# Kernel tuning notes

Hardware: AMD Instinct MI355X
Metric: run time of the kernel (lower is better)

Reference implementation:

```python
import jax, jax.numpy as jnp
import numpy as np

B, S, E, H = 2, 2048, 1024, 16
D = E // H  # head_dim = 64


def setup_inputs() -> dict:
    key = jax.random.key(0)
    ks = jax.random.split(key, 8)
    lim = float(np.sqrt(6.0 / (E + E)))  # xavier_uniform
    inp = {
        "query": jax.random.normal(ks[0], (B, S, E), jnp.float32),
        "key": jax.random.normal(ks[1], (B, S, E), jnp.float32),
        "value": jax.random.normal(ks[2], (B, S, E), jnp.float32),
        "Wq": jax.random.uniform(ks[3], (E, E), jnp.float32, -lim, lim),
        "Wk": jax.random.uniform(ks[4], (E, E), jnp.float32, -lim, lim),
        "Wv": jax.random.uniform(ks[5], (E, E), jnp.float32, -lim, lim),
        "Wo": jax.random.uniform(ks[6], (E, E), jnp.float32, -lim, lim),
        "bq": jnp.zeros((E,), jnp.float32),
        "bk": jnp.zeros((E,), jnp.float32),
        "bv": jnp.zeros((E,), jnp.float32),
        "bo": jnp.zeros((E,), jnp.float32),
        # causal mask: True = masked (strictly upper triangular)
        "attn_mask": jnp.triu(jnp.ones((S, S), jnp.bool_), k=1),
    }
    return inp


def reference(query, key, value, Wq, Wk, Wv, Wo, bq, bk, bv, bo, attn_mask):
    # W stored as (in, out); torch Linear equivalent y = x @ W + b
    scaling = D ** (-0.5)
    q = (query @ Wq + bq) * scaling            # (B,S,E), first scaling (MHA.forward)
    k = key @ Wk + bk
    v = value @ Wv + bv
    # split heads -> (B, H, S, D)
    q = q.reshape(B, S, H, D).transpose(0, 2, 1, 3)
    k = k.reshape(B, S, H, D).transpose(0, 2, 1, 3)
    v = v.reshape(B, S, H, D).transpose(0, 2, 1, 3)
    # second scaling inside ScaledDotProductAttention (faithful double-scale)
    scores = jnp.einsum("bhqd,bhkd->bhqk", q, k) / jnp.sqrt(jnp.float32(D))
    scores = jnp.where(attn_mask[None, None, :, :], -jnp.inf, scores)
    attn = jax.nn.softmax(scores, axis=-1)     # dropout is identity in eval
    out = jnp.einsum("bhqk,bhkd->bhqd", attn, v)
    out = out.transpose(0, 2, 1, 3).reshape(B, S, E)
    return out @ Wo + bo
```

## Files before the change

kernel.cpp:

```cpp
#include <hip/hip_runtime.h>
#include <stdint.h>

#define B_ 2
#define S_ 2048
#define E_ 1024
#define H_ 16
#define D_ 64

typedef __attribute__((ext_vector_type(8))) short bf16x8;
typedef __attribute__((ext_vector_type(4))) float f32x4;
typedef __attribute__((ext_vector_type(4))) short s16x4_t;

__device__ __forceinline__ short bfbits(float x) {
    union { float f; uint32_t u; } v; v.f = x;
    uint32_t r = v.u + 0x7fffu + ((v.u >> 16) & 1u);
    return (short)(r >> 16);
}
__device__ __forceinline__ short bfbits_trunc(float x) {
    union { float f; uint32_t u; } v; v.f = x;
    return (short)(v.u >> 16);
}

__device__ __forceinline__ void async16(const short* g, short* l) {
    __builtin_amdgcn_global_load_lds((const __attribute__((address_space(1))) void*)g,
                                     (__attribute__((address_space(3))) void*)l,
                                     16, 0, 0);
}

__global__ __launch_bounds__(256) void cvt_all(const float* __restrict__ q,
                                               const float* __restrict__ k,
                                               const float* __restrict__ v,
                                               const float* __restrict__ Wq,
                                               const float* __restrict__ Wk,
                                               const float* __restrict__ Wv,
                                               const float* __restrict__ Wo,
                                               short* __restrict__ dstX,
                                               short* __restrict__ dstW) {
    __shared__ short t[64][72];
    int bid = blockIdx.x;
    if (bid < 12288) {
        const long long NV = 1048576;
        long long i = (long long)bid * 256 + threadIdx.x;
        const float* src = (i < NV) ? q : (i < 2 * NV) ? k : v;
        long long j = (i >= 2 * NV) ? (i - 2 * NV) : (i >= NV) ? (i - NV) : i;
        float4 x = ((const float4*)src)[j];
        s16x4_t o;
        o[0] = bfbits(x.x); o[1] = bfbits(x.y); o[2] = bfbits(x.z); o[3] = bfbits(x.w);
        ((s16x4_t*)dstX)[i] = o;
        return;
    }
    int wbid = bid - 12288;
    int z = wbid >> 8;
    const float* W = (z == 0) ? Wq : (z == 1) ? Wk : (z == 2) ? Wv : Wo;
    short* o = dstW + (size_t)z * 1048576;
    int rem = wbid & 255;
    int n0 = (rem & 15) * 64, k0 = (rem >> 4) * 64;
    int tid = threadIdx.x;
    int r = tid >> 4, c4 = tid & 15;
    for (int rep = 0; rep < 4; rep++) {
        int kk = rep * 16 + r;
        float4 x = *(const float4*)&W[(size_t)(k0 + kk) * 1024 + n0 + c4 * 4];
        t[c4 * 4 + 0][kk] = bfbits(x.x);
        t[c4 * 4 + 1][kk] = bfbits(x.y);
        t[c4 * 4 + 2][kk] = bfbits(x.z);
        t[c4 * 4 + 3][kk] = bfbits(x.w);
    }
    __syncthreads();
    int n = tid >> 3, c8 = tid & 7;
    for (int rep = 0; rep < 2; rep++) {
        int nn = rep * 32 + n;
        bf16x8 vv;
        for (int jj = 0; jj < 8; jj++) vv[jj] = t[nn][c8 * 8 + jj];
        *(bf16x8*)&o[(size_t)(n0 + nn) * 1024 + k0 + c8 * 8] = vv;
    }
}

__device__ __forceinline__ void gemm_core(const short* __restrict__ A,
                                          const short* __restrict__ Bt,
                                          const float* __restrict__ bias,
                                          short* __restrict__ outB,
                                          float* __restrict__ outF,
                                          int mode, float scale,
                                          int m0, int n0) {
    __shared__ short As[2][128 * 32];
    __shared__ short Bs[2][128 * 32];
    int tid = threadIdx.x, lane = tid & 63, w = tid >> 6;
    int col = lane & 15, quad = lane >> 4;
    int wm = (w >> 1) * 64, wn = (w & 1) * 64;
    f32x4 acc[4][4];
    for (int i = 0; i < 4; i++)
        for (int j = 0; j < 4; j++) acc[i][j] = (f32x4){0.f, 0.f, 0.f, 0.f};

    int r4 = lane >> 2;
    int skoff = ((lane & 3) ^ ((r4 >> 1) & 3)) * 8;
    const short* ga = A + (size_t)(m0 + r4) * 1024 + skoff;
    const short* gb = Bt + (size_t)(n0 + r4) * 1024 + skoff;

    int fro = (quad ^ ((col >> 1) & 3)) * 8;

    auto stage = [&](int t, int b) {
        int k0_ = t * 32;
        for (int c = 0; c < 2; ++c) {
            int rb = w * 32 + c * 16;
            async16(ga + (size_t)rb * 1024 + k0_, &As[b][rb * 32]);
            async16(gb + (size_t)rb * 1024 + k0_, &Bs[b][rb * 32]);
        }
    };

    stage(0, 0);
    __syncthreads();
    for (int t = 0; t < 32; ++t) {
        int cur = t & 1;
        if (t + 1 < 32) stage(t + 1, cur ^ 1);
        bf16x8 af[4], bfr[4];
        for (int i = 0; i < 4; i++)
            af[i] = *(const bf16x8*)&As[cur][(wm + i * 16 + col) * 32 + fro];
        for (int j = 0; j < 4; j++)
            bfr[j] = *(const bf16x8*)&Bs[cur][(wn + j * 16 + col) * 32 + fro];
        for (int i = 0; i < 4; i++)
            for (int j = 0; j < 4; j++)
                acc[i][j] = __builtin_amdgcn_mfma_f32_16x16x32_bf16(af[i], bfr[j], acc[i][j], 0, 0, 0);
        __syncthreads();
    }

    int mbase = m0 + wm + quad * 4;
    for (int i = 0; i < 4; i++) {
        int mb = mbase + i * 16;
        for (int j = 0; j < 4; j++) {
            int n = n0 + wn + j * 16 + col;
            float bv_ = bias[n];
            if (mode == 0) {
                for (int r = 0; r < 4; r++)
                    outB[(size_t)(mb + r) * 1024 + n] = bfbits((acc[i][j][r] + bv_) * scale);
            } else if (mode == 1) {
                int b_ = mb >> 11, s_ = mb & 2047;
                size_t base = (((size_t)(b_ * 16 + (n >> 6)) * 64) + (n & 63)) * 2048 + s_;
                s16x4_t pv;
                for (int r = 0; r < 4; r++) pv[r] = bfbits((acc[i][j][r] + bv_) * scale);
                *(s16x4_t*)&outB[base] = pv;
            } else {
                for (int r = 0; r < 4; r++)
                    outF[(size_t)(mb + r) * 1024 + n] = (acc[i][j][r] + bv_) * scale;
            }
        }
    }
}

#define QSCALE (0.015625f * 1.44269504088896340736f)
__global__ __launch_bounds__(256) void gemm_qkv(const short* __restrict__ Xb,
                                                const short* __restrict__ Wb,
                                                const float* __restrict__ bq,
                                                const float* __restrict__ bk,
                                                const float* __restrict__ bv,
                                                short* __restrict__ Qp) {
    int bid = blockIdx.x;
    int L = (bid & 7) * 96 + (bid >> 3);
    int z = L >> 8;
    int rem = L & 255;
    int m0 = (rem >> 3) * 128, n0 = (rem & 7) * 128;
    const short* A = Xb + (size_t)z * 4194304;
    const short* Bt = Wb + (size_t)z * 1048576;
    const float* bias = (z == 0) ? bq : (z == 1) ? bk : bv;
    short* outB = Qp + (size_t)z * 4194304;
    gemm_core(A, Bt, bias, outB, nullptr, (z == 2) ? 1 : 0, (z == 0) ? QSCALE : 1.0f,
              m0, n0);
}

__global__ __launch_bounds__(256) void gemm_o(const short* __restrict__ Ctx,
                                              const short* __restrict__ Wob,
                                              const float* __restrict__ bo,
                                              float* __restrict__ out) {
    int bid = blockIdx.x;
    int L = (bid & 7) * 32 + (bid >> 3);
    int m0 = (L >> 3) * 128, n0 = (L & 7) * 128;
    gemm_core(Ctx, Wob, bo, nullptr, out, 2, 1.0f, m0, n0);
}

__device__ __forceinline__ void stage_kv(const short* __restrict__ Kp,
                                         const short* __restrict__ VpT,
                                         short* Kbuf, short* Vbuf,
                                         int b, int bh, int h, int kv0,
                                         int lane, int w) {
    int r8 = lane >> 3;
    int sk = ((lane & 7) ^ r8) * 8;
    for (int c = 0; c < 2; c++) {
        int rb = (c * 4 + w) * 8;
        async16(Kp + (size_t)(b * 2048 + kv0 + rb + r8) * 1024 + h * 64 + sk,
                &Kbuf[rb * 64]);
        async16(VpT + (size_t)(bh * 64 + rb + r8) * 2048 + kv0 + sk,
                &Vbuf[rb * 64]);
    }
}

__global__ __launch_bounds__(256) void attn_kernel(const short* __restrict__ Qp,
                                                   const short* __restrict__ Kp,
                                                   const short* __restrict__ VpT,
                                                   short* __restrict__ Ctx) {
    __shared__ short Kt[2][64 * 64];
    __shared__ short Vt[2][64 * 64];
    __shared__ short Pl[4][16 * 72];
    int tid = threadIdx.x, lane = tid & 63, w = tid >> 6;
    int col = lane & 15, quad = lane >> 4;
    int c7 = col & 7;
    int bid = blockIdx.x;
    int L = (bid & 7) * 128 + (bid >> 3);
    int bh = L >> 5;
    int qt = 31 - (L & 31);
    int b = bh >> 4, h = bh & 15;
    int qrow = qt * 64 + w * 16;

    bf16x8 ones;
    for (int j = 0; j < 8; j++) ones[j] = (short)0x3F80;

    bf16x8 aq0, aq1;
    {
        const short* qa = Qp + ((size_t)(b * 2048 + qrow + col)) * 1024 + h * 64;
        aq0 = *(const bf16x8*)(qa + quad * 8);
        aq1 = *(const bf16x8*)(qa + 32 + quad * 8);
    }
    f32x4 o[4];
    for (int dj = 0; dj < 4; dj++) o[dj] = (f32x4){0.f, 0.f, 0.f, 0.f};
    f32x4 psv = (f32x4){0.f, 0.f, 0.f, 0.f};

    int n = qt + 1;
    stage_kv(Kp, VpT, Kt[0], Vt[0], b, bh, h, 0, lane, w);

    for (int t = 0; t < n; t++) {
        __syncthreads();
        if (t + 1 < n)
            stage_kv(Kp, VpT, Kt[(t + 1) & 1], Vt[(t + 1) & 1], b, bh, h,
                     (t + 1) * 64, lane, w);
        const short* Kb = Kt[t & 1];
        const short* Vb = Vt[t & 1];

        f32x4 sf[4];
        for (int i = 0; i < 4; i++) sf[i] = (f32x4){0.f, 0.f, 0.f, 0.f};
        __builtin_amdgcn_s_setprio(1);
        for (int ks = 0; ks < 2; ks++) {
            bf16x8 bq_ = ks ? aq1 : aq0;
            int sl = ((ks * 4 + quad) ^ c7) * 8;
            for (int i = 0; i < 4; i++) {
                bf16x8 ak_ = *(const bf16x8*)&Kb[(i * 16 + col) * 64 + sl];
                sf[i] = __builtin_amdgcn_mfma_f32_16x16x32_bf16(ak_, bq_, sf[i], 0, 0, 0);
            }
        }
        __builtin_amdgcn_s_setprio(0);
        if (t == n - 1) {
            int qg = qrow + col;
            for (int i = 0; i < 4; i++) {
                int kvg = t * 64 + i * 16 + quad * 4;
                for (int r = 0; r < 4; r++)
                    if (kvg + r > qg) sf[i][r] = -3.0e38f;
            }
        }
        for (int i = 0; i < 4; i++) {
            s16x4_t pw;
            for (int r = 0; r < 4; r++)
                pw[r] = bfbits_trunc(exp2f(sf[i][r]));
            *(s16x4_t*)&Pl[w][col * 72 + i * 16 + quad * 4] = pw;
        }
        __builtin_amdgcn_s_setprio(1);
        for (int ks = 0; ks < 2; ks++) {
            bf16x8 ap = *(const bf16x8*)&Pl[w][col * 72 + ks * 32 + quad * 8];
            int sl = ((ks * 4 + quad) ^ c7) * 8;
            psv = __builtin_amdgcn_mfma_f32_16x16x32_bf16(ap, ones, psv, 0, 0, 0);
            for (int dj = 0; dj < 4; dj++) {
                bf16x8 bv_ = *(const bf16x8*)&Vb[(dj * 16 + col) * 64 + sl];
                o[dj] = __builtin_amdgcn_mfma_f32_16x16x32_bf16(ap, bv_, o[dj], 0, 0, 0);
            }
        }
        __builtin_amdgcn_s_setprio(0);
    }
    float inv[4];
    for (int r = 0; r < 4; r++) inv[r] = 1.0f / psv[r];
    for (int r = 0; r < 4; r++) {
        for (int dj = 0; dj < 4; dj++) {
            float val = o[dj][r] * inv[r];
            Ctx[((size_t)(b * 2048 + qrow + quad * 4 + r)) * 1024 + h * 64 + dj * 16 + col] = bfbits(val);
        }
    }
}

extern "C" void kernel_launch(void* const* d_in, const int* in_sizes, int n_in,
                              void* d_out, int out_size, void* d_ws, size_t ws_size,
                              hipStream_t stream) {
    const float* q  = (const float*)d_in[0];
    const float* k  = (const float*)d_in[1];
    const float* v  = (const float*)d_in[2];
    const float* Wq = (const float*)d_in[3];
    const float* Wk = (const float*)d_in[4];
    const float* Wv = (const float*)d_in[5];
    const float* Wo = (const float*)d_in[6];
    const float* bq = (const float*)d_in[7];
    const float* bk = (const float*)d_in[8];
    const float* bv = (const float*)d_in[9];
    const float* bo = (const float*)d_in[10];

    short* wsb = (short*)d_ws;
    short* Wb  = wsb;
    short* Xb  = Wb + 4 * 1048576;
    short* Qp  = Xb + 3 * 4194304;
    short* Kp  = Qp + 4194304;
    short* VpT = Kp + 4194304;
    short* Ctx = VpT + 4194304;

    cvt_all<<<13312, 256, 0, stream>>>(q, k, v, Wq, Wk, Wv, Wo, Xb, Wb);
    gemm_qkv<<<768, 256, 0, stream>>>(Xb, Wb, bq, bk, bv, Qp);
    attn_kernel<<<1024, 256, 0, stream>>>(Qp, Kp, VpT, Ctx);
    gemm_o<<<256, 256, 0, stream>>>(Ctx, Wb + 3 * 1048576, bo, (float*)d_out);
}
```

Baseline: 245.3 us.

## Pair causal query tiles per block to balance work and share KV tiles

Each attention block now handles two query tiles, qx and 31-qx, from the same head. The short tile reuses the same staged K/V tiles as the long one, so every block does equal causal work and loads each K/V tile once for both. The grid is halved to 512 blocks and per-thread register use roughly doubles (two accumulator sets), which may reduce occupancy.

```diff
diff --git a/kernel.cpp b/kernel.cpp
--- a/kernel.cpp
+++ b/kernel.cpp
@@ -95,7 +95,6 @@
     int skoff = ((lane & 3) ^ ((r4 >> 1) & 3)) * 8;
     const short* ga = A + (size_t)(m0 + r4) * 1024 + skoff;
     const short* gb = Bt + (size_t)(n0 + r4) * 1024 + skoff;
-
     int fro = (quad ^ ((col >> 1) & 3)) * 8;
 
     auto stage = [&](int t, int b) {
@@ -198,85 +197,158 @@
                                                    short* __restrict__ Ctx) {
     __shared__ short Kt[2][64 * 64];
     __shared__ short Vt[2][64 * 64];
-    __shared__ short Pl[4][16 * 72];
+    __shared__ short Pl[8][16 * 72];
     int tid = threadIdx.x, lane = tid & 63, w = tid >> 6;
     int col = lane & 15, quad = lane >> 4;
     int c7 = col & 7;
     int bid = blockIdx.x;
-    int L = (bid & 7) * 128 + (bid >> 3);
-    int bh = L >> 5;
-    int qt = 31 - (L & 31);
+    int L = (bid & 7) * 64 + (bid >> 3);
+    int qx = L & 15, bh = L >> 4;
     int b = bh >> 4, h = bh & 15;
-    int qrow = qt * 64 + w * 16;
+    int qtA = qx, qtB = 31 - qx;
+    int nA = qtA + 1, nB = qtB + 1;
+    int qrowA = qtA * 64 + w * 16, qrowB = qtB * 64 + w * 16;
 
     bf16x8 ones;
     for (int j = 0; j < 8; j++) ones[j] = (short)0x3F80;
 
-    bf16x8 aq0, aq1;
+    bf16x8 aqA0, aqA1, aqB0, aqB1;
     {
-        const short* qa = Qp + ((size_t)(b * 2048 + qrow + col)) * 1024 + h * 64;
-        aq0 = *(const bf16x8*)(qa + quad * 8);
-        aq1 = *(const bf16x8*)(qa + 32 + quad * 8);
-    }
-    f32x4 o[4];
-    for (int dj = 0; dj < 4; dj++) o[dj] = (f32x4){0.f, 0.f, 0.f, 0.f};
-    f32x4 psv = (f32x4){0.f, 0.f, 0.f, 0.f};
-
-    int n = qt + 1;
+        const short* qa = Qp + ((size_t)(b * 2048 + qrowA + col)) * 1024 + h * 64;
+        aqA0 = *(const bf16x8*)(qa + quad * 8);
+        aqA1 = *(const bf16x8*)(qa + 32 + quad * 8);
+        const short* qb = Qp + ((size_t)(b * 2048 + qrowB + col)) * 1024 + h * 64;
+        aqB0 = *(const bf16x8*)(qb + quad * 8);
+        aqB1 = *(const bf16x8*)(qb + 32 + quad * 8);
+    }
+    f32x4 oA[4], oB[4];
+    for (int dj = 0; dj < 4; dj++) {
+        oA[dj] = (f32x4){0.f, 0.f, 0.f, 0.f};
+        oB[dj] = (f32x4){0.f, 0.f, 0.f, 0.f};
+    }
+    f32x4 psvA = (f32x4){0.f, 0.f, 0.f, 0.f};
+    f32x4 psvB = (f32x4){0.f, 0.f, 0.f, 0.f};
+
+    short* PlA = Pl[w * 2];
+    short* PlB = Pl[w * 2 + 1];
+
     stage_kv(Kp, VpT, Kt[0], Vt[0], b, bh, h, 0, lane, w);
 
-    for (int t = 0; t < n; t++) {
+    int t = 0;
+    for (; t < nA; ++t) {
         __syncthreads();
-        if (t + 1 < n)
+        stage_kv(Kp, VpT, Kt[(t + 1) & 1], Vt[(t + 1) & 1], b, bh, h,
+                 (t + 1) * 64, lane, w);
+        const short* Kb = Kt[t & 1];
+        const short* Vb = Vt[t & 1];
+
+        f32x4 sfA[4], sfB[4];
+        for (int i = 0; i < 4; i++) {
+            sfA[i] = (f32x4){0.f, 0.f, 0.f, 0.f};
+            sfB[i] = (f32x4){0.f, 0.f, 0.f, 0.f};
+        }
+        __builtin_amdgcn_s_setprio(1);
+        for (int ks = 0; ks < 2; ks++) {
+            bf16x8 bqA = ks ? aqA1 : aqA0;
+            bf16x8 bqB = ks ? aqB1 : aqB0;
+            int sl = ((ks * 4 + quad) ^ c7) * 8;
+            for (int i = 0; i < 4; i++) {
+                bf16x8 ak_ = *(const bf16x8*)&Kb[(i * 16 + col) * 64 + sl];
+                sfB[i] = __builtin_amdgcn_mfma_f32_16x16x32_bf16(ak_, bqB, sfB[i], 0, 0, 0);
+                sfA[i] = __builtin_amdgcn_mfma_f32_16x16x32_bf16(ak_, bqA, sfA[i], 0, 0, 0);
+            }
+        }
+        __builtin_amdgcn_s_setprio(0);
+        if (t == nA - 1) {
+            int qg = qrowA + col;
+            for (int i = 0; i < 4; i++) {
+                int kvg = t * 64 + i * 16 + quad * 4;
+                for (int r = 0; r < 4; r++)
+                    if (kvg + r > qg) sfA[i][r] = -3.0e38f;
+            }
+        }
+        for (int i = 0; i < 4; i++) {
+            s16x4_t pw;
+            for (int r = 0; r < 4; r++) pw[r] = bfbits_trunc(exp2f(sfB[i][r]));
+            *(s16x4_t*)&PlB[col * 72 + i * 16 + quad * 4] = pw;
+        }
+        for (int i = 0; i < 4; i++) {
+            s16x4_t pw;
+            for (int r = 0; r < 4; r++) pw[r] = bfbits_trunc(exp2f(sfA[i][r]));
+            *(s16x4_t*)&PlA[col * 72 + i * 16 + quad * 4] = pw;
+        }
+        __builtin_amdgcn_s_setprio(1);
+        for (int ks = 0; ks < 2; ks++) {
+            bf16x8 apB = *(const bf16x8*)&PlB[col * 72 + ks * 32 + quad * 8];
+            bf16x8 apA = *(const bf16x8*)&PlA[col * 72 + ks * 32 + quad * 8];
+            int sl = ((ks * 4 + quad) ^ c7) * 8;
+            psvB = __builtin_amdgcn_mfma_f32_16x16x32_bf16(apB, ones, psvB, 0, 0, 0);
+            psvA = __builtin_amdgcn_mfma_f32_16x16x32_bf16(apA, ones, psvA, 0, 0, 0);
+            for (int dj = 0; dj < 4; dj++) {
+                bf16x8 bv_ = *(const bf16x8*)&Vb[(dj * 16 + col) * 64 + sl];
+                oB[dj] = __builtin_amdgcn_mfma_f32_16x16x32_bf16(apB, bv_, oB[dj], 0, 0, 0);
+                oA[dj] = __builtin_amdgcn_mfma_f32_16x16x32_bf16(apA, bv_, oA[dj], 0, 0, 0);
+            }
+        }
+        __builtin_amdgcn_s_setprio(0);
+    }
+    for (; t < nB; ++t) {
+        __syncthreads();
+        if (t + 1 < nB)
             stage_kv(Kp, VpT, Kt[(t + 1) & 1], Vt[(t + 1) & 1], b, bh, h,
                      (t + 1) * 64, lane, w);
         const short* Kb = Kt[t & 1];
         const short* Vb = Vt[t & 1];
 
-        f32x4 sf[4];
-        for (int i = 0; i < 4; i++) sf[i] = (f32x4){0.f, 0.f, 0.f, 0.f};
+        f32x4 sfB[4];
+        for (int i = 0; i < 4; i++) sfB[i] = (f32x4){0.f, 0.f, 0.f, 0.f};
         __builtin_amdgcn_s_setprio(1);
         for (int ks = 0; ks < 2; ks++) {
-            bf16x8 bq_ = ks ? aq1 : aq0;
+            bf16x8 bqB = ks ? aqB1 : aqB0;
             int sl = ((ks * 4 + quad) ^ c7) * 8;
             for (int i = 0; i < 4; i++) {
                 bf16x8 ak_ = *(const bf16x8*)&Kb[(i * 16 + col) * 64 + sl];
-                sf[i] = __builtin_amdgcn_mfma_f32_16x16x32_bf16(ak_, bq_, sf[i], 0, 0, 0);
+                sfB[i] = __builtin_amdgcn_mfma_f32_16x16x32_bf16(ak_, bqB, sfB[i], 0, 0, 0);
             }
         }
         __builtin_amdgcn_s_setprio(0);
-        if (t == n - 1) {
-            int qg = qrow + col;
+        if (t == nB - 1) {
+            int qg = qrowB + col;
             for (int i = 0; i < 4; i++) {
                 int kvg = t * 64 + i * 16 + quad * 4;
                 for (int r = 0; r < 4; r++)
-                    if (kvg + r > qg) sf[i][r] = -3.0e38f;
+                    if (kvg + r > qg) sfB[i][r] = -3.0e38f;
             }
         }
         for (int i = 0; i < 4; i++) {
             s16x4_t pw;
-            for (int r = 0; r < 4; r++)
-                pw[r] = bfbits_trunc(exp2f(sf[i][r]));
-            *(s16x4_t*)&Pl[w][col * 72 + i * 16 + quad * 4] = pw;
+            for (int r = 0; r < 4; r++) pw[r] = bfbits_trunc(exp2f(sfB[i][r]));
+            *(s16x4_t*)&PlB[col * 72 + i * 16 + quad * 4] = pw;
         }
         __builtin_amdgcn_s_setprio(1);
         for (int ks = 0; ks < 2; ks++) {
-            bf16x8 ap = *(const bf16x8*)&Pl[w][col * 72 + ks * 32 + quad * 8];
+            bf16x8 apB = *(const bf16x8*)&PlB[col * 72 + ks * 32 + quad * 8];
             int sl = ((ks * 4 + quad) ^ c7) * 8;
-            psv = __builtin_amdgcn_mfma_f32_16x16x32_bf16(ap, ones, psv, 0, 0, 0);
+            psvB = __builtin_amdgcn_mfma_f32_16x16x32_bf16(apB, ones, psvB, 0, 0, 0);
             for (int dj = 0; dj < 4; dj++) {
                 bf16x8 bv_ = *(const bf16x8*)&Vb[(dj * 16 + col) * 64 + sl];
-                o[dj] = __builtin_amdgcn_mfma_f32_16x16x32_bf16(ap, bv_, o[dj], 0, 0, 0);
+                oB[dj] = __builtin_amdgcn_mfma_f32_16x16x32_bf16(apB, bv_, oB[dj], 0, 0, 0);
             }
         }
         __builtin_amdgcn_s_setprio(0);
     }
-    float inv[4];
-    for (int r = 0; r < 4; r++) inv[r] = 1.0f / psv[r];
+
+    float invA[4], invB[4];
+    for (int r = 0; r < 4; r++) {
+        invA[r] = 1.0f / psvA[r];
+        invB[r] = 1.0f / psvB[r];
+    }
     for (int r = 0; r < 4; r++) {
         for (int dj = 0; dj < 4; dj++) {
-            float val = o[dj][r] * inv[r];
-            Ctx[((size_t)(b * 2048 + qrow + quad * 4 + r)) * 1024 + h * 64 + dj * 16 + col] = bfbits(val);
+            Ctx[((size_t)(b * 2048 + qrowA + quad * 4 + r)) * 1024 + h * 64 + dj * 16 + col] =
+                bfbits(oA[dj][r] * invA[r]);
+            Ctx[((size_t)(b * 2048 + qrowB + quad * 4 + r)) * 1024 + h * 64 + dj * 16 + col] =
+                bfbits(oB[dj][r] * invB[r]);
         }
     }
 }
@@ -306,6 +378,6 @@
 
     cvt_all<<<13312, 256, 0, stream>>>(q, k, v, Wq, Wk, Wv, Wo, Xb, Wb);
     gemm_qkv<<<768, 256, 0, stream>>>(Xb, Wb, bq, bk, bv, Qp);
-    attn_kernel<<<1024, 256, 0, stream>>>(Qp, Kp, VpT, Ctx);
+    attn_kernel<<<512, 256, 0, stream>>>(Qp, Kp, VpT, Ctx);
     gemm_o<<<256, 256, 0, stream>>>(Ctx, Wb + 3 * 1048576, bo, (float*)d_out);
 }
```

New measurement: 240.3 us. 2.1% less time.

## Pair complementary causal query tiles in one 512-thread attention block

Applied to the files above, without the earlier changes.

Each attention block now holds 8 waves: four handle query tile qx and four handle the mirrored tile 31-qx. The K/V tiles for the longer tile are staged once into shared memory and reused by both halves. This evens out causal load imbalance across blocks and removes duplicate K/V loads for the shorter tile. In exchange, the waves on the short tile sit idle at the barriers for the remaining iterations, and the larger blocks with half the block count may change occupancy.

```diff
diff --git a/kernel.cpp b/kernel.cpp
--- a/kernel.cpp
+++ b/kernel.cpp
@@ -95,7 +95,6 @@
     int skoff = ((lane & 3) ^ ((r4 >> 1) & 3)) * 8;
     const short* ga = A + (size_t)(m0 + r4) * 1024 + skoff;
     const short* gb = Bt + (size_t)(n0 + r4) * 1024 + skoff;
-
     int fro = (quad ^ ((col >> 1) & 3)) * 8;
 
     auto stage = [&](int t, int b) {
@@ -176,38 +175,37 @@
     gemm_core(Ctx, Wob, bo, nullptr, out, 2, 1.0f, m0, n0);
 }
 
-__device__ __forceinline__ void stage_kv(const short* __restrict__ Kp,
-                                         const short* __restrict__ VpT,
-                                         short* Kbuf, short* Vbuf,
-                                         int b, int bh, int h, int kv0,
-                                         int lane, int w) {
-    int r8 = lane >> 3;
-    int sk = ((lane & 7) ^ r8) * 8;
-    for (int c = 0; c < 2; c++) {
-        int rb = (c * 4 + w) * 8;
-        async16(Kp + (size_t)(b * 2048 + kv0 + rb + r8) * 1024 + h * 64 + sk,
-                &Kbuf[rb * 64]);
-        async16(VpT + (size_t)(bh * 64 + rb + r8) * 2048 + kv0 + sk,
-                &Vbuf[rb * 64]);
-    }
-}
-
-__global__ __launch_bounds__(256) void attn_kernel(const short* __restrict__ Qp,
+__device__ __forceinline__ void stage_kv8(const short* __restrict__ Kp,
+                                          const short* __restrict__ VpT,
+                                          short* Kbuf, short* Vbuf,
+                                          int b, int bh, int h, int kv0,
+                                          int tid) {
+    int row = tid >> 3;
+    int sk = ((tid & 7) ^ (row & 7)) * 8;
+    int wbase = (tid >> 6) * 512;
+    async16(Kp + (size_t)(b * 2048 + kv0 + row) * 1024 + h * 64 + sk, &Kbuf[wbase]);
+    async16(VpT + (size_t)(bh * 64 + row) * 2048 + kv0 + sk, &Vbuf[wbase]);
+}
+
+__global__ __launch_bounds__(512) void attn_kernel(const short* __restrict__ Qp,
                                                    const short* __restrict__ Kp,
                                                    const short* __restrict__ VpT,
                                                    short* __restrict__ Ctx) {
     __shared__ short Kt[2][64 * 64];
     __shared__ short Vt[2][64 * 64];
-    __shared__ short Pl[4][16 * 72];
+    __shared__ short Pl[8][16 * 72];
     int tid = threadIdx.x, lane = tid & 63, w = tid >> 6;
     int col = lane & 15, quad = lane >> 4;
     int c7 = col & 7;
     int bid = blockIdx.x;
-    int L = (bid & 7) * 128 + (bid >> 3);
-    int bh = L >> 5;
-    int qt = 31 - (L & 31);
+    int L = (bid & 7) * 64 + (bid >> 3);
+    int qx = L & 15, bh = L >> 4;
     int b = bh >> 4, h = bh & 15;
-    int qrow = qt * 64 + w * 16;
+    int wi = w & 3;
+    int qt = (w < 4) ? qx : (31 - qx);
+    int myN = qt + 1;
+    int nB = 32 - qx;
+    int qrow = qt * 64 + wi * 16;
 
     bf16x8 ones;
     for (int j = 0; j < 8; j++) ones[j] = (short)0x3F80;
@@ -222,54 +220,57 @@
     for (int dj = 0; dj < 4; dj++) o[dj] = (f32x4){0.f, 0.f, 0.f, 0.f};
     f32x4 psv = (f32x4){0.f, 0.f, 0.f, 0.f};
 
-    int n = qt + 1;
-    stage_kv(Kp, VpT, Kt[0], Vt[0], b, bh, h, 0, lane, w);
-
-    for (int t = 0; t < n; t++) {
+    short* Plw = Pl[w];
+
+    stage_kv8(Kp, VpT, Kt[0], Vt[0], b, bh, h, 0, tid);
+
+    for (int t = 0; t < nB; t++) {
         __syncthreads();
-        if (t + 1 < n)
-            stage_kv(Kp, VpT, Kt[(t + 1) & 1], Vt[(t + 1) & 1], b, bh, h,
-                     (t + 1) * 64, lane, w);
-        const short* Kb = Kt[t & 1];
-        const short* Vb = Vt[t & 1];
-
-        f32x4 sf[4];
-        for (int i = 0; i < 4; i++) sf[i] = (f32x4){0.f, 0.f, 0.f, 0.f};
-        __builtin_amdgcn_s_setprio(1);
-        for (int ks = 0; ks < 2; ks++) {
-            bf16x8 bq_ = ks ? aq1 : aq0;
-            int sl = ((ks * 4 + quad) ^ c7) * 8;
+        if (t + 1 < nB)
+            stage_kv8(Kp, VpT, Kt[(t + 1) & 1], Vt[(t + 1) & 1], b, bh, h,
+                      (t + 1) * 64, tid);
+        if (t < myN) {
+            const short* Kb = Kt[t & 1];
+            const short* Vb = Vt[t & 1];
+
+            f32x4 sf[4];
+            for (int i = 0; i < 4; i++) sf[i] = (f32x4){0.f, 0.f, 0.f, 0.f};
+            __builtin_amdgcn_s_setprio(1);
+            for (int ks = 0; ks < 2; ks++) {
+                bf16x8 bq_ = ks ? aq1 : aq0;
+                int sl = ((ks * 4 + quad) ^ c7) * 8;
+                for (int i = 0; i < 4; i++) {
+                    bf16x8 ak_ = *(const bf16x8*)&Kb[(i * 16 + col) * 64 + sl];
+                    sf[i] = __builtin_amdgcn_mfma_f32_16x16x32_bf16(ak_, bq_, sf[i], 0, 0, 0);
+                }
+            }
+            __builtin_amdgcn_s_setprio(0);
+            if (t == myN - 1) {
+                int qg = qrow + col;
+                for (int i = 0; i < 4; i++) {
+                    int kvg = t * 64 + i * 16 + quad * 4;
+                    for (int r = 0; r < 4; r++)
+                        if (kvg + r > qg) sf[i][r] = -3.0e38f;
+                }
+            }
             for (int i = 0; i < 4; i++) {
-                bf16x8 ak_ = *(const bf16x8*)&Kb[(i * 16 + col) * 64 + sl];
-                sf[i] = __builtin_amdgcn_mfma_f32_16x16x32_bf16(ak_, bq_, sf[i], 0, 0, 0);
-            }
+                s16x4_t pw;
+                for (int r = 0; r < 4; r++)
+                    pw[r] = bfbits_trunc(exp2f(sf[i][r]));
+                *(s16x4_t*)&Plw[col * 72 + i * 16 + quad * 4] = pw;
+            }
+            __builtin_amdgcn_s_setprio(1);
+            for (int ks = 0; ks < 2; ks++) {
+                bf16x8 ap = *(const bf16x8*)&Plw[col * 72 + ks * 32 + quad * 8];
+                int sl = ((ks * 4 + quad) ^ c7) * 8;
+                psv = __builtin_amdgcn_mfma_f32_16x16x32_bf16(ap, ones, psv, 0, 0, 0);
+                for (int dj = 0; dj < 4; dj++) {
+                    bf16x8 bv_ = *(const bf16x8*)&Vb[(dj * 16 + col) * 64 + sl];
+                    o[dj] = __builtin_amdgcn_mfma_f32_16x16x32_bf16(ap, bv_, o[dj], 0, 0, 0);
+                }
+            }
+            __builtin_amdgcn_s_setprio(0);
         }
-        __builtin_amdgcn_s_setprio(0);
-        if (t == n - 1) {
-            int qg = qrow + col;
-            for (int i = 0; i < 4; i++) {
-                int kvg = t * 64 + i * 16 + quad * 4;
-                for (int r = 0; r < 4; r++)
-                    if (kvg + r > qg) sf[i][r] = -3.0e38f;
-            }
-        }
-        for (int i = 0; i < 4; i++) {
-            s16x4_t pw;
-            for (int r = 0; r < 4; r++)
-                pw[r] = bfbits_trunc(exp2f(sf[i][r]));
-            *(s16x4_t*)&Pl[w][col * 72 + i * 16 + quad * 4] = pw;
-        }
-        __builtin_amdgcn_s_setprio(1);
-        for (int ks = 0; ks < 2; ks++) {
-            bf16x8 ap = *(const bf16x8*)&Pl[w][col * 72 + ks * 32 + quad * 8];
-            int sl = ((ks * 4 + quad) ^ c7) * 8;
-            psv = __builtin_amdgcn_mfma_f32_16x16x32_bf16(ap, ones, psv, 0, 0, 0);
-            for (int dj = 0; dj < 4; dj++) {
-                bf16x8 bv_ = *(const bf16x8*)&Vb[(dj * 16 + col) * 64 + sl];
-                o[dj] = __builtin_amdgcn_mfma_f32_16x16x32_bf16(ap, bv_, o[dj], 0, 0, 0);
-            }
-        }
-        __builtin_amdgcn_s_setprio(0);
     }
     float inv[4];
     for (int r = 0; r < 4; r++) inv[r] = 1.0f / psv[r];
@@ -306,6 +307,6 @@
 
     cvt_all<<<13312, 256, 0, stream>>>(q, k, v, Wq, Wk, Wv, Wo, Xb, Wb);
     gemm_qkv<<<768, 256, 0, stream>>>(Xb, Wb, bq, bk, bv, Qp);
-    attn_kernel<<<1024, 256, 0, stream>>>(Qp, Kp, VpT, Ctx);
+    attn_kernel<<<512, 512, 0, stream>>>(Qp, Kp, VpT, Ctx);
     gemm_o<<<256, 256, 0, stream>>>(Ctx, Wb + 3 * 1048576, bo, (float*)d_out);
 }
```

After: 243.8 us. About the same (-0.6%).
